# Optimization experiments

Hardware: AMD Instinct MI355X
Metric: run time of the kernel (lower is better)

The kernel has to match this reference:

```python
import jax, jax.numpy as jnp
import numpy as np

EPS = 1e-5  # PyTorch BatchNorm2d default eps


def _batchnorm(x, gamma, beta):
    # training-mode BN over (N, T, V) per channel; x: [N, C, T, V]
    mean = jnp.mean(x, axis=(0, 2, 3), keepdims=True)
    var = jnp.var(x, axis=(0, 2, 3), keepdims=True)
    inv = jax.lax.rsqrt(var + EPS)
    return (x - mean) * inv * gamma[None, :, None, None] + beta[None, :, None, None]


def setup_inputs() -> dict:
    key = jax.random.key(0)
    ks = jax.random.split(key, 8)
    N, Cin, Cout, T, V, S = 64, 64, 128, 300, 25, 3
    x = jax.random.normal(ks[0], (N, Cin, T, V), dtype=jnp.float32)
    A = jax.random.uniform(ks[1], (S, V, V), dtype=jnp.float32)
    # per-subset 1x1 conv weights/biases (kaiming-ish scale)
    W = jax.random.normal(ks[2], (S, Cout, Cin), dtype=jnp.float32) / np.sqrt(Cin)
    b = jax.random.normal(ks[3], (S, Cout), dtype=jnp.float32) * 0.01
    alpha = jnp.zeros((1,), dtype=jnp.float32)
    bn_gamma = jnp.ones((Cout,), dtype=jnp.float32)
    bn_beta = jnp.zeros((Cout,), dtype=jnp.float32)
    # residual down path (in_channels != out_channels): conv1x1 + BN
    down_W = jax.random.normal(ks[4], (Cout, Cin), dtype=jnp.float32) / np.sqrt(Cin)
    down_b = jax.random.normal(ks[5], (Cout,), dtype=jnp.float32) * 0.01
    down_gamma = jnp.ones((Cout,), dtype=jnp.float32)
    down_beta = jnp.zeros((Cout,), dtype=jnp.float32)
    return {
        "x": x, "A": A, "W": W, "b": b, "alpha": alpha,
        "bn_gamma": bn_gamma, "bn_beta": bn_beta,
        "down_W": down_W, "down_b": down_b,
        "down_gamma": down_gamma, "down_beta": down_beta,
    }


def reference(x, A, W, b, alpha, bn_gamma, bn_beta, down_W, down_b, down_gamma, down_beta):
    V = x.shape[-1]
    eye = jnp.eye(V, dtype=x.dtype)
    A_adj = A + alpha[0] * eye[None]  # [S, V, V]
    # sum_s conv1x1_s( x @ A_s ): fuse adjacency matmul, 1x1 conv, subset sum
    y_agg = jnp.einsum('nctv,svw,soc->notw', x, A_adj, W)
    y_agg = y_agg + jnp.sum(b, axis=0)[None, :, None, None]
    y = _batchnorm(y_agg, bn_gamma, bn_beta)
    # residual down: 1x1 conv + BN (in_channels != out_channels)
    res = jnp.einsum('nctv,oc->notv', x, down_W) + down_b[None, :, None, None]
    res = _batchnorm(res, down_gamma, down_beta)
    return jax.nn.relu(y + res)
```

## Files before the change

kernel.cpp:

```cpp
#include <hip/hip_runtime.h>
#include <hip/hip_bf16.h>

#define N_   64
#define CIN  64
#define COUT 128
#define T_   300
#define V_   25
#define S_   3
#define NTV  (N_ * T_ * V_)

#define TS     10
#define NTB    (T_ / TS)
#define NBLK   (N_ * NTB)
#define RED_ROWS   64
#define RED_BLOCKS (NBLK / RED_ROWS)

#define WS_P    0
#define WS_P2   (WS_P + NBLK * 512)
#define WS_COEF (WS_P2 + RED_BLOCKS * 512)
#define WS_WF   (WS_COEF + 512)
#define WS_WSF  (WS_WF + 16384)
#define WS_AF   (WS_WSF + 16384)

typedef __attribute__((ext_vector_type(8))) short short8;
typedef __attribute__((ext_vector_type(4))) float f32x4;

__device__ __forceinline__ unsigned short bfbits(float f) {
    union { __hip_bfloat16 h; unsigned short u; } cv;
    cv.h = __float2bfloat16(f);
    return cv.u;
}

__device__ __forceinline__ int zoff(int nl, int k) {
    int slot = (k >> 3) ^ (nl & 31);
    return nl * 512 + slot * 16 + (k & 7) * 2;
}

__global__ __launch_bounds__(256) void k_prep(const float* __restrict__ W,
                                              const float* __restrict__ dW,
                                              const float* __restrict__ A,
                                              const float* __restrict__ alpha,
                                              unsigned short* __restrict__ Wf,
                                              unsigned short* __restrict__ Af) {
    int i = blockIdx.x * 256 + threadIdx.x;
    {
        int j = i & 7, lane = (i >> 3) & 63, ks = (i >> 9) & 7;
        int of = (i >> 12) & 1, oh = i >> 13;
        int lq = lane >> 4, lr = lane & 15;
        int o = oh * 32 + of * 16 + lr;
        int k = ks * 32 + lq * 8 + j;
        float wv = (k < 192) ? W[(k >> 6) * (COUT * CIN) + o * CIN + (k & 63)]
                             : dW[o * CIN + (k - 192)];
        Wf[i] = bfbits(wv);
    }
    if (i < 3072) {
        int j = i & 7, lane = (i >> 3) & 63, wf = (i >> 9) & 1, s = i >> 10;
        int lq = lane >> 4, lr = lane & 15;
        int v = lq * 8 + j, w = wf * 16 + lr;
        float av = (v < V_ && w < V_)
                     ? A[(s * V_ + v) * V_ + w] + ((v == w) ? alpha[0] : 0.f)
                     : 0.f;
        Af[i] = bfbits(av);
    }
}

__global__ __launch_bounds__(256) void k_prep2(const float* __restrict__ W,
                                               const float* __restrict__ dW,
                                               const float* __restrict__ coef,
                                               unsigned short* __restrict__ Wsf) {
    int i = blockIdx.x * 256 + threadIdx.x;
    int j = i & 7, lane = (i >> 3) & 63, ks = (i >> 9) & 7;
    int of = (i >> 12) & 1, oh = i >> 13;
    int lq = lane >> 4, lr = lane & 15;
    int o = oh * 32 + of * 16 + lr;
    int k = ks * 32 + lq * 8 + j;
    float wv = (k < 192) ? W[(k >> 6) * (COUT * CIN) + o * CIN + (k & 63)]
                         : dW[o * CIN + (k - 192)];
    float sc = (k < 192) ? coef[o] : coef[COUT + o];
    Wsf[i] = bfbits(wv * sc);
    (void)j;
}

__device__ __forceinline__ void stage(char* zb, const unsigned short* Alds,
                                      f32x4 a0, f32x4 a1, float x24,
                                      int oh, int lq, int lr, int lane)
{
    const bool q3 = (lq == 3);
    float f[8];
    f[0] = q3 ? x24 : a0[0];
    f[1] = q3 ? 0.f : a0[1];
    f[2] = q3 ? 0.f : a0[2];
    f[3] = q3 ? 0.f : a0[3];
    f[4] = q3 ? 0.f : a1[0];
    f[5] = q3 ? 0.f : a1[1];
    f[6] = q3 ? 0.f : a1[2];
    f[7] = q3 ? 0.f : a1[3];

    short8 xfr;
    const int kc = 192 + oh * 16 + lr;
#pragma unroll
    for (int j = 0; j < 8; ++j) {
        unsigned short e = bfbits(f[j]);
        xfr[j] = (short)e;
        *(unsigned short*)(zb + zoff(lq * 8 + j, kc)) = e;
    }

    const f32x4 zero = {0.f, 0.f, 0.f, 0.f};
    const int kc2 = oh * 16 + lr;
#pragma unroll
    for (int s = 0; s < S_; ++s)
#pragma unroll
        for (int wf = 0; wf < 2; ++wf) {
            short8 af = *(const short8*)(Alds + ((s * 2 + wf) * 64 + lane) * 8);
            f32x4 d = __builtin_amdgcn_mfma_f32_16x16x32_bf16(af, xfr, zero, 0, 0, 0);
#pragma unroll
            for (int r = 0; r < 4; ++r)
                *(unsigned short*)(zb + zoff(wf * 16 + lq * 4 + r, s * 64 + kc2)) = bfbits(d[r]);
        }
}

template<bool STATS>
__global__ __launch_bounds__(256, 3) void k_gemm(
    const float* __restrict__ x, const unsigned short* __restrict__ Wf,
    const unsigned short* __restrict__ Af, const float* __restrict__ coef,
    float* __restrict__ P, float* __restrict__ out)
{
    __shared__ __align__(16) unsigned short Zt[2][32 * 256];
    __shared__ __align__(16) unsigned short Alds[6 * 64 * 8];

    const int tid = threadIdx.x;
    const int oh = tid >> 6, lane = tid & 63;
    const int lq = lane >> 4, lr = lane & 15;

    const int bid = blockIdx.x;
    const int n = bid / NTB, tb = bid % NTB;
    const int t0 = tb * TS;

    for (int i = tid; i < 384; i += 256)
        *(short8*)(Alds + i * 8) = *(const short8*)(Af + i * 8);

    short8 wfr[2][8];
#pragma unroll
    for (int of = 0; of < 2; ++of)
#pragma unroll
        for (int ks = 0; ks < 8; ++ks)
            wfr[of][ks] = *(const short8*)(Wf + (((oh * 2 + of) * 8 + ks) * 64 + lane) * 8);

    float c0v[2] = {0.f, 0.f};
    if (!STATS) {
        c0v[0] = coef[2 * COUT + oh * 32 + lr];
        c0v[1] = coef[2 * COUT + oh * 32 + 16 + lr];
    }

    float sy[2] = {0.f, 0.f}, sy2[2] = {0.f, 0.f};
    float sr[2] = {0.f, 0.f}, sr2[2] = {0.f, 0.f};

    const int c = oh * 16 + lr;
    const float* xrow = x + ((size_t)(n * CIN + c) * T_) * V_;
    const int vb = (lq < 3) ? lq * 8 : 16;

    __syncthreads();

    {
        const float* base = xrow + (size_t)t0 * V_;
        f32x4 a0 = *(const f32x4*)(base + vb);
        f32x4 a1 = *(const f32x4*)(base + vb + 4);
        float x24 = base[24];
        stage((char*)Zt[0], Alds, a0, a1, x24, oh, lq, lr, lane);
    }

    const f32x4 zero = {0.f, 0.f, 0.f, 0.f};

    for (int tt = 0; tt < TS; ++tt) {
        const int t = t0 + tt;
        char* zb = (char*)Zt[tt & 1];
        __syncthreads();

        f32x4 pa0 = zero, pa1 = zero; float px24 = 0.f;
        if (tt + 1 < TS) {
            const float* base = xrow + (size_t)(t + 1) * V_;
            pa0 = *(const f32x4*)(base + vb);
            pa1 = *(const f32x4*)(base + vb + 4);
            px24 = base[24];
        }

        f32x4 acc[2][2], accr[2][2];
#pragma unroll
        for (int ks = 0; ks < 8; ++ks) {
            short8 za[2];
            za[0] = *(const short8*)(zb + zoff(lr, ks * 32 + lq * 8));
            za[1] = *(const short8*)(zb + zoff(16 + lr, ks * 32 + lq * 8));
            if constexpr (STATS) {
                if (ks < 6) {
#pragma unroll
                    for (int mf = 0; mf < 2; ++mf)
#pragma unroll
                        for (int of = 0; of < 2; ++of)
                            acc[mf][of] = __builtin_amdgcn_mfma_f32_16x16x32_bf16(
                                za[mf], wfr[of][ks], ks == 0 ? zero : acc[mf][of], 0, 0, 0);
                } else {
#pragma unroll
                    for (int mf = 0; mf < 2; ++mf)
#pragma unroll
                        for (int of = 0; of < 2; ++of)
                            accr[mf][of] = __builtin_amdgcn_mfma_f32_16x16x32_bf16(
                                za[mf], wfr[of][ks], ks == 6 ? zero : accr[mf][of], 0, 0, 0);
                }
            } else {
#pragma unroll
                for (int mf = 0; mf < 2; ++mf)
#pragma unroll
                    for (int of = 0; of < 2; ++of)
                        acc[mf][of] = __builtin_amdgcn_mfma_f32_16x16x32_bf16(
                            za[mf], wfr[of][ks], ks == 0 ? zero : acc[mf][of], 0, 0, 0);
            }
        }

        if (tt + 1 < TS)
            stage((char*)Zt[(tt + 1) & 1], Alds, pa0, pa1, px24, oh, lq, lr, lane);

        if constexpr (STATS) {
#pragma unroll
            for (int of = 0; of < 2; ++of)
#pragma unroll
                for (int mf = 0; mf < 2; ++mf)
#pragma unroll
                    for (int r = 0; r < 4; ++r) {
                        float yv = acc[mf][of][r];
                        sy[of] += yv; sy2[of] = fmaf(yv, yv, sy2[of]);
                        float rv = accr[mf][of][r];
                        sr[of] += rv; sr2[of] = fmaf(rv, rv, sr2[of]);
                    }
        } else {
#pragma unroll
            for (int of = 0; of < 2; ++of) {
                int o = oh * 32 + of * 16 + lr;
                float* rowp = out + ((size_t)(n * COUT + o) * T_ + t) * V_;
                f32x4 v0;
#pragma unroll
                for (int r = 0; r < 4; ++r) v0[r] = fmaxf(acc[0][of][r] + c0v[of], 0.f);
                *(f32x4*)(rowp + lq * 4) = v0;
                if (lq < 2) {
                    f32x4 v1;
#pragma unroll
                    for (int r = 0; r < 4; ++r) v1[r] = fmaxf(acc[1][of][r] + c0v[of], 0.f);
                    *(f32x4*)(rowp + 16 + lq * 4) = v1;
                } else if (lq == 2) {
                    rowp[24] = fmaxf(acc[1][of][0] + c0v[of], 0.f);
                }
            }
        }
    }

    if constexpr (STATS) {
#pragma unroll
        for (int of = 0; of < 2; ++of) {
            sy[of]  += __shfl_xor(sy[of], 16);  sy[of]  += __shfl_xor(sy[of], 32);
            sy2[of] += __shfl_xor(sy2[of], 16); sy2[of] += __shfl_xor(sy2[of], 32);
            sr[of]  += __shfl_xor(sr[of], 16);  sr[of]  += __shfl_xor(sr[of], 32);
            sr2[of] += __shfl_xor(sr2[of], 16); sr2[of] += __shfl_xor(sr2[of], 32);
        }
        if (lq == 0) {
            float* p = P + (size_t)bid * 512;
#pragma unroll
            for (int of = 0; of < 2; ++of) {
                int o = oh * 32 + of * 16 + lr;
                p[o] = sy[of]; p[128 + o] = sy2[of];
                p[256 + o] = sr[of]; p[384 + o] = sr2[of];
            }
        }
    }
}

__global__ __launch_bounds__(256) void k_red(const float* __restrict__ P,
                                             float* __restrict__ P2) {
    const int tid = threadIdx.x;
    float a0 = 0.f, a1 = 0.f;
    const int row0 = blockIdx.x * RED_ROWS;
    for (int r = 0; r < RED_ROWS; ++r) {
        const float* p = P + (size_t)(row0 + r) * 512;
        a0 += p[tid];
        a1 += p[256 + tid];
    }
    P2[blockIdx.x * 512 + tid] = a0;
    P2[blockIdx.x * 512 + 256 + tid] = a1;
}

__global__ __launch_bounds__(128) void k_coef(
    const float* __restrict__ P2, const float* __restrict__ gamma,
    const float* __restrict__ beta, const float* __restrict__ dgamma,
    const float* __restrict__ dbeta, const float* __restrict__ b,
    const float* __restrict__ db, float* __restrict__ coef) {
    const int o = threadIdx.x;
    float sy = 0.f, sy2 = 0.f, sr = 0.f, sr2 = 0.f;
    for (int r2 = 0; r2 < RED_BLOCKS; ++r2) {
        const float* p = P2 + r2 * 512;
        sy += p[o]; sy2 += p[128 + o]; sr += p[256 + o]; sr2 += p[384 + o];
    }
    const float bsum = b[o] + b[COUT + o] + b[2 * COUT + o];
    const float dbo = db[o];
    float syb  = sy + (float)NTV * bsum;
    float sy2b = sy2 + 2.f * bsum * sy + (float)NTV * bsum * bsum;
    float srb  = sr + (float)NTV * dbo;
    float sr2b = sr2 + 2.f * dbo * sr + (float)NTV * dbo * dbo;
    const float invn = 1.f / (float)NTV;
    float my = syb * invn, mr = srb * invn;
    float vy = fmaf(-my, my, sy2b * invn);
    float vr = fmaf(-mr, mr, sr2b * invn);
    float ay = rsqrtf(vy + 1e-5f) * gamma[o];
    float ar = rsqrtf(vr + 1e-5f) * dgamma[o];
    float c0 = beta[o] - my * ay + dbeta[o] - mr * ar + ay * bsum + ar * dbo;
    coef[o] = ay; coef[COUT + o] = ar; coef[2 * COUT + o] = c0;
}

extern "C" void kernel_launch(void* const* d_in, const int* in_sizes, int n_in,
                              void* d_out, int out_size, void* d_ws, size_t ws_size,
                              hipStream_t stream) {
    const float* x      = (const float*)d_in[0];
    const float* A      = (const float*)d_in[1];
    const float* W      = (const float*)d_in[2];
    const float* b      = (const float*)d_in[3];
    const float* alpha  = (const float*)d_in[4];
    const float* gamma  = (const float*)d_in[5];
    const float* beta   = (const float*)d_in[6];
    const float* dW     = (const float*)d_in[7];
    const float* db     = (const float*)d_in[8];
    const float* dgamma = (const float*)d_in[9];
    const float* dbeta  = (const float*)d_in[10];

    float* ws   = (float*)d_ws;
    float* P    = ws + WS_P;
    float* P2   = ws + WS_P2;
    float* coef = ws + WS_COEF;
    unsigned short* Wf  = (unsigned short*)(ws + WS_WF);
    unsigned short* Wsf = (unsigned short*)(ws + WS_WSF);
    unsigned short* Af  = (unsigned short*)(ws + WS_AF);
    float* out  = (float*)d_out;

    k_prep<<<128, 256, 0, stream>>>(W, dW, A, alpha, Wf, Af);
    k_gemm<true><<<NBLK, 256, 0, stream>>>(x, Wf, Af, nullptr, P, nullptr);
    k_red<<<RED_BLOCKS, 256, 0, stream>>>(P, P2);
    k_coef<<<1, 128, 0, stream>>>(P2, gamma, beta, dgamma, dbeta, b, db, coef);
    k_prep2<<<128, 256, 0, stream>>>(W, dW, coef, Wsf);
    k_gemm<false><<<NBLK, 256, 0, stream>>>(x, Wsf, Af, coef, nullptr, out);
}
```

Before: 249.1 us.

## Swap MFMA operand order in staging, keep adjacency in registers, shrink time tile

The staging step now puts x in the MFMA A operand and the adjacency in B. Each lane's outputs then land on contiguous K positions and are written to LDS as packed 64-bit stores instead of many 16-bit scattered stores. The residual x slice is produced by a fourth identity 'subset' MFMA rather than separate per-element LDS writes. Adjacency fragments are held in registers instead of LDS, which removes an initial barrier, and the time tile per block drops from 10 to 6 to launch more blocks. The costs are extra MFMA work, more register pressure, and more partial-stat blocks to reduce.

```diff
diff --git a/kernel.cpp b/kernel.cpp
--- a/kernel.cpp
+++ b/kernel.cpp
@@ -9,7 +9,7 @@
 #define S_   3
 #define NTV  (N_ * T_ * V_)
 
-#define TS     10
+#define TS     6
 #define NTB    (T_ / TS)
 #define NBLK   (N_ * NTB)
 #define RED_ROWS   64
@@ -29,6 +29,9 @@
     union { __hip_bfloat16 h; unsigned short u; } cv;
     cv.h = __float2bfloat16(f);
     return cv.u;
+}
+__device__ __forceinline__ unsigned int pack2(float lo, float hi) {
+    return (unsigned int)bfbits(lo) | ((unsigned int)bfbits(hi) << 16);
 }
 
 __device__ __forceinline__ int zoff(int nl, int k) {
@@ -46,20 +49,22 @@
     {
         int j = i & 7, lane = (i >> 3) & 63, ks = (i >> 9) & 7;
         int of = (i >> 12) & 1, oh = i >> 13;
-        int lq = lane >> 4, lr = lane & 15;
-        int o = oh * 32 + of * 16 + lr;
-        int k = ks * 32 + lq * 8 + j;
+        int o = oh * 32 + of * 16 + (lane & 15);
+        int k = ks * 32 + (lane >> 4) * 8 + j;
         float wv = (k < 192) ? W[(k >> 6) * (COUT * CIN) + o * CIN + (k & 63)]
                              : dW[o * CIN + (k - 192)];
         Wf[i] = bfbits(wv);
     }
-    if (i < 3072) {
+    if (i < 4096) {
         int j = i & 7, lane = (i >> 3) & 63, wf = (i >> 9) & 1, s = i >> 10;
-        int lq = lane >> 4, lr = lane & 15;
-        int v = lq * 8 + j, w = wf * 16 + lr;
-        float av = (v < V_ && w < V_)
-                     ? A[(s * V_ + v) * V_ + w] + ((v == w) ? alpha[0] : 0.f)
-                     : 0.f;
+        int v = (lane >> 4) * 8 + j, w = wf * 16 + (lane & 15);
+        float av;
+        if (s < 3)
+            av = (v < V_ && w < V_)
+                   ? A[(s * V_ + v) * V_ + w] + ((v == w) ? alpha[0] : 0.f)
+                   : 0.f;
+        else
+            av = (v == w && v < V_) ? 1.f : 0.f;
         Af[i] = bfbits(av);
     }
 }
@@ -71,51 +76,46 @@
     int i = blockIdx.x * 256 + threadIdx.x;
     int j = i & 7, lane = (i >> 3) & 63, ks = (i >> 9) & 7;
     int of = (i >> 12) & 1, oh = i >> 13;
-    int lq = lane >> 4, lr = lane & 15;
-    int o = oh * 32 + of * 16 + lr;
-    int k = ks * 32 + lq * 8 + j;
+    int o = oh * 32 + of * 16 + (lane & 15);
+    int k = ks * 32 + (lane >> 4) * 8 + j;
     float wv = (k < 192) ? W[(k >> 6) * (COUT * CIN) + o * CIN + (k & 63)]
                          : dW[o * CIN + (k - 192)];
     float sc = (k < 192) ? coef[o] : coef[COUT + o];
     Wsf[i] = bfbits(wv * sc);
-    (void)j;
-}
-
-__device__ __forceinline__ void stage(char* zb, const unsigned short* Alds,
-                                      f32x4 a0, f32x4 a1, float x24,
-                                      int oh, int lq, int lr, int lane)
-{
-    const bool q3 = (lq == 3);
-    float f[8];
-    f[0] = q3 ? x24 : a0[0];
-    f[1] = q3 ? 0.f : a0[1];
-    f[2] = q3 ? 0.f : a0[2];
-    f[3] = q3 ? 0.f : a0[3];
-    f[4] = q3 ? 0.f : a1[0];
-    f[5] = q3 ? 0.f : a1[1];
-    f[6] = q3 ? 0.f : a1[2];
-    f[7] = q3 ? 0.f : a1[3];
-
-    short8 xfr;
-    const int kc = 192 + oh * 16 + lr;
-#pragma unroll
-    for (int j = 0; j < 8; ++j) {
-        unsigned short e = bfbits(f[j]);
-        xfr[j] = (short)e;
-        *(unsigned short*)(zb + zoff(lq * 8 + j, kc)) = e;
-    }
-
+}
+
+__device__ __forceinline__ short8 load_xfr(const float* __restrict__ base, int lq) {
+    short8 r;
+    if (lq < 3) {
+        f32x4 a0 = *(const f32x4*)(base + lq * 8);
+        f32x4 a1 = *(const f32x4*)(base + lq * 8 + 4);
+#pragma unroll
+        for (int j = 0; j < 4; ++j) {
+            r[j]     = (short)bfbits(a0[j]);
+            r[4 + j] = (short)bfbits(a1[j]);
+        }
+    } else {
+        float v = base[24];
+        r[0] = (short)bfbits(v);
+#pragma unroll
+        for (int j = 1; j < 8; ++j) r[j] = 0;
+    }
+    return r;
+}
+
+__device__ __forceinline__ void stage(char* zb, const short8* af, short8 xfr,
+                                      int oh, int lq, int lr) {
     const f32x4 zero = {0.f, 0.f, 0.f, 0.f};
-    const int kc2 = oh * 16 + lr;
-#pragma unroll
-    for (int s = 0; s < S_; ++s)
+#pragma unroll
+    for (int s = 0; s < 4; ++s)
 #pragma unroll
         for (int wf = 0; wf < 2; ++wf) {
-            short8 af = *(const short8*)(Alds + ((s * 2 + wf) * 64 + lane) * 8);
-            f32x4 d = __builtin_amdgcn_mfma_f32_16x16x32_bf16(af, xfr, zero, 0, 0, 0);
-#pragma unroll
-            for (int r = 0; r < 4; ++r)
-                *(unsigned short*)(zb + zoff(wf * 16 + lq * 4 + r, s * 64 + kc2)) = bfbits(d[r]);
+            f32x4 d = __builtin_amdgcn_mfma_f32_16x16x32_bf16(xfr, af[s * 2 + wf], zero, 0, 0, 0);
+            unsigned long long pk = (unsigned long long)pack2(d[0], d[1])
+                                  | ((unsigned long long)pack2(d[2], d[3]) << 32);
+            int row = wf * 16 + lr;
+            int k = s * 64 + oh * 16 + lq * 4;
+            *(unsigned long long*)(zb + zoff(row, k)) = pk;
         }
 }
 
@@ -126,7 +126,6 @@
     float* __restrict__ P, float* __restrict__ out)
 {
     __shared__ __align__(16) unsigned short Zt[2][32 * 256];
-    __shared__ __align__(16) unsigned short Alds[6 * 64 * 8];
 
     const int tid = threadIdx.x;
     const int oh = tid >> 6, lane = tid & 63;
@@ -136,8 +135,10 @@
     const int n = bid / NTB, tb = bid % NTB;
     const int t0 = tb * TS;
 
-    for (int i = tid; i < 384; i += 256)
-        *(short8*)(Alds + i * 8) = *(const short8*)(Af + i * 8);
+    short8 af[8];
+#pragma unroll
+    for (int i = 0; i < 8; ++i)
+        af[i] = *(const short8*)(Af + (i * 64 + lane) * 8);
 
     short8 wfr[2][8];
 #pragma unroll
@@ -157,16 +158,10 @@
 
     const int c = oh * 16 + lr;
     const float* xrow = x + ((size_t)(n * CIN + c) * T_) * V_;
-    const int vb = (lq < 3) ? lq * 8 : 16;
-
-    __syncthreads();
 
     {
-        const float* base = xrow + (size_t)t0 * V_;
-        f32x4 a0 = *(const f32x4*)(base + vb);
-        f32x4 a1 = *(const f32x4*)(base + vb + 4);
-        float x24 = base[24];
-        stage((char*)Zt[0], Alds, a0, a1, x24, oh, lq, lr, lane);
+        short8 xf0 = load_xfr(xrow + (size_t)t0 * V_, lq);
+        stage((char*)Zt[0], af, xf0, oh, lq, lr);
     }
 
     const f32x4 zero = {0.f, 0.f, 0.f, 0.f};
@@ -176,13 +171,8 @@
         char* zb = (char*)Zt[tt & 1];
         __syncthreads();
 
-        f32x4 pa0 = zero, pa1 = zero; float px24 = 0.f;
-        if (tt + 1 < TS) {
-            const float* base = xrow + (size_t)(t + 1) * V_;
-            pa0 = *(const f32x4*)(base + vb);
-            pa1 = *(const f32x4*)(base + vb + 4);
-            px24 = base[24];
-        }
+        short8 nxfr;
+        if (tt + 1 < TS) nxfr = load_xfr(xrow + (size_t)(t + 1) * V_, lq);
 
         f32x4 acc[2][2], accr[2][2];
 #pragma unroll
@@ -217,7 +207,7 @@
         }
 
         if (tt + 1 < TS)
-            stage((char*)Zt[(tt + 1) & 1], Alds, pa0, pa1, px24, oh, lq, lr, lane);
+            stage((char*)Zt[(tt + 1) & 1], af, nxfr, oh, lq, lr);
 
         if constexpr (STATS) {
 #pragma unroll
```

After: 500.3 us. 2.01x slower.
